# Kernel tuning notes

Measured on AMD Instinct MI355X. Metric: run time of the kernel, lower is better.

The kernel has to match this reference:

```python
import jax, jax.numpy as jnp
import numpy as np

H = 1024       # hidden_size
E = 1024       # embedding_size
V = 50257      # output_size (vocab)
L = 64         # max_length


def setup_inputs() -> dict:
    key = jax.random.key(0)
    ks = jax.random.split(key, 12)
    s = 0.02
    return {
        "input": jax.random.randint(ks[0], (1,), 0, V),
        "hidden": jax.random.normal(ks[1], (1, 1, H), dtype=jnp.float32),
        "encoder_outputs": jax.random.normal(ks[2], (L, H), dtype=jnp.float32),
        "emb": jax.random.normal(ks[3], (V, E), dtype=jnp.float32) * s,
        "attn_w": jax.random.normal(ks[4], (L, H + E), dtype=jnp.float32) * s,
        "attn_b": jnp.zeros((L,), dtype=jnp.float32),
        "comb_w": jax.random.normal(ks[5], (E, H + E), dtype=jnp.float32) * s,
        "comb_b": jnp.zeros((E,), dtype=jnp.float32),
        "w_ih": jax.random.normal(ks[6], (3 * H, E), dtype=jnp.float32) * s,
        "b_ih": jnp.zeros((3 * H,), dtype=jnp.float32),
        "w_hh": jax.random.normal(ks[7], (3 * H, H), dtype=jnp.float32) * s,
        "b_hh": jnp.zeros((3 * H,), dtype=jnp.float32),
        "out_w": jax.random.normal(ks[8], (V, H), dtype=jnp.float32) * s,
        "out_b": jnp.zeros((V,), dtype=jnp.float32),
    }


def reference(input, hidden, encoder_outputs, emb, attn_w, attn_b,
              comb_w, comb_b, w_ih, b_ih, w_hh, b_hh, out_w, out_b):
    # embedding + (dropout = identity in eval)
    embedded = emb[input].reshape(1, E)            # [1, E]
    h0 = hidden[0]                                  # [1, H]
    # Bahdanau-style attention over fixed-length encoder outputs
    attn_logits = jnp.concatenate([embedded, h0], axis=1) @ attn_w.T + attn_b
    attn_weights = jax.nn.softmax(attn_logits, axis=1)      # [1, L]
    attn_applied = attn_weights @ encoder_outputs            # [1, H]
    x = jnp.concatenate([embedded, attn_applied], axis=1) @ comb_w.T + comb_b
    x = jax.nn.relu(x)                               # [1, E]
    # single GRU cell step (torch gate order: r, z, n)
    gi = x @ w_ih.T + b_ih
    gh = h0 @ w_hh.T + b_hh
    i_r, i_z, i_n = jnp.split(gi, 3, axis=1)
    h_r, h_z, h_n = jnp.split(gh, 3, axis=1)
    r = jax.nn.sigmoid(i_r + h_r)
    z = jax.nn.sigmoid(i_z + h_z)
    n = jnp.tanh(i_n + r * h_n)
    h_new = (1.0 - z) * n + z * h0                   # [1, H]
    logp = jax.nn.log_softmax(h_new @ out_w.T + out_b, axis=1)  # [1, V]
    return logp, h_new[None], attn_weights
```

## Files before the change

### kernel.cpp

```cpp
#include <hip/hip_runtime.h>
#include <math.h>

#define H 1024
#define E 1024
#define V 50257
#define L 64
#define HE 2048

__device__ inline float wave_reduce_sum(float v) {
    #pragma unroll
    for (int off = 32; off > 0; off >>= 1)
        v += __shfl_down(v, off, 64);
    return v;
}

__device__ inline float wave_allreduce_sum(float v) {
    #pragma unroll
    for (int off = 32; off > 0; off >>= 1)
        v += __shfl_xor(v, off, 64);
    return v;
}

__device__ inline void ms_merge(float& M, float& S, float m2, float s2) {
    if (s2 > 0.f) {
        if (m2 > M) { S = S * expf(M - m2) + s2; M = m2; }
        else        { S += s2 * expf(m2 - M); }
    }
}

__global__ __launch_bounds__(1024) void k_attn_fused(
        const int* __restrict__ inp,
        const float* __restrict__ hidden,
        const float* __restrict__ emb,
        const float* __restrict__ attn_w,
        const float* __restrict__ attn_b,
        const float* __restrict__ enc,
        float* __restrict__ attn_applied,
        float* __restrict__ out_weights) {
    __shared__ float lg[L];
    __shared__ float wsm[L];
    int t = threadIdx.x;
    int wave = t >> 6, lane = t & 63;
    const float* erow = emb + (size_t)inp[0] * E;
    const float4* e4 = (const float4*)erow;
    const float4* h4 = (const float4*)hidden;
    #pragma unroll
    for (int r = wave; r < L; r += 16) {
        const float4* w = (const float4*)(attn_w + (size_t)r * HE);
        float s = 0.f;
        #pragma unroll
        for (int i = 0; i < 4; ++i) {
            float4 wv = w[i * 64 + lane];
            float4 ev = e4[i * 64 + lane];
            s += wv.x*ev.x + wv.y*ev.y + wv.z*ev.z + wv.w*ev.w;
        }
        #pragma unroll
        for (int i = 0; i < 4; ++i) {
            float4 wv = w[256 + i * 64 + lane];
            float4 hv = h4[i * 64 + lane];
            s += wv.x*hv.x + wv.y*hv.y + wv.z*hv.z + wv.w*hv.w;
        }
        s = wave_reduce_sum(s);
        if (lane == 0) lg[r] = s + attn_b[r];
    }
    __syncthreads();
    if (t < 64) {
        float v = lg[t];
        float m = v;
        #pragma unroll
        for (int off = 32; off > 0; off >>= 1) m = fmaxf(m, __shfl_xor(m, off, 64));
        float ex = expf(v - m);
        float ssum = ex;
        #pragma unroll
        for (int off = 32; off > 0; off >>= 1) ssum += __shfl_xor(ssum, off, 64);
        float w = ex / ssum;
        wsm[t] = w;
        out_weights[t] = w;
    }
    __syncthreads();
    float acc = 0.f;
    #pragma unroll 16
    for (int l = 0; l < L; ++l)
        acc += wsm[l] * enc[l * H + t];
    attn_applied[t] = acc;
}

__global__ __launch_bounds__(256) void k_comb(
        const int* __restrict__ inp,
        const float* __restrict__ emb,
        const float* __restrict__ attn_applied,
        const float* __restrict__ comb_w,
        const float* __restrict__ comb_b,
        float* __restrict__ x) {
    int t = threadIdx.x, wave = t >> 6, lane = t & 63;
    int row  = blockIdx.x * 2 + (wave >> 1);
    int half = wave & 1;
    const float* erow = emb + (size_t)inp[0] * E;
    const float4* vec = half ? (const float4*)attn_applied : (const float4*)erow;
    const float4* w = (const float4*)(comb_w + (size_t)row * HE + half * E);
    float s = 0.f;
    #pragma unroll
    for (int i = 0; i < 4; ++i) {
        float4 wv = w[i * 64 + lane];
        float4 vv = vec[i * 64 + lane];
        s += wv.x*vv.x + wv.y*vv.y + wv.z*vv.z + wv.w*vv.w;
    }
    s = wave_reduce_sum(s);
    __shared__ float red[4];
    if (lane == 0) red[wave] = s;
    __syncthreads();
    if (t < 2) {
        int r = blockIdx.x * 2 + t;
        x[r] = fmaxf(red[2 * t] + red[2 * t + 1] + comb_b[r], 0.f);
    }
}

__global__ __launch_bounds__(384) void k_gru(
        const float* __restrict__ x,
        const float* __restrict__ hidden,
        const float* __restrict__ w_ih,
        const float* __restrict__ b_ih,
        const float* __restrict__ w_hh,
        const float* __restrict__ b_hh,
        float* __restrict__ h_new) {
    int t = threadIdx.x, wave = t >> 6, lane = t & 63;
    int j = blockIdx.x;
    const float* W    = (wave < 3) ? w_ih : w_hh;
    const float* vsrc = (wave < 3) ? x    : hidden;
    int g = (wave < 3) ? wave : wave - 3;
    const float4* wr = (const float4*)(W + (size_t)(g * H + j) * H);
    const float4* v4 = (const float4*)vsrc;
    float s = 0.f;
    #pragma unroll
    for (int i = 0; i < 4; ++i) {
        float4 wv = wr[i * 64 + lane];
        float4 vv = v4[i * 64 + lane];
        s += wv.x*vv.x + wv.y*vv.y + wv.z*vv.z + wv.w*vv.w;
    }
    s = wave_reduce_sum(s);
    __shared__ float red[6];
    if (lane == 0) red[wave] = s;
    __syncthreads();
    if (t == 0) {
        float i_r = red[0] + b_ih[j];
        float i_z = red[1] + b_ih[H + j];
        float i_n = red[2] + b_ih[2 * H + j];
        float h_r = red[3] + b_hh[j];
        float h_z = red[4] + b_hh[H + j];
        float h_n = red[5] + b_hh[2 * H + j];
        float r = 1.f / (1.f + expf(-(i_r + h_r)));
        float z = 1.f / (1.f + expf(-(i_z + h_z)));
        float n = tanhf(i_n + r * h_n);
        h_new[j] = (1.f - z) * n + z * hidden[j];
    }
}

__global__ __launch_bounds__(256) void k_outproj(
        const float* __restrict__ h_new,
        const float* __restrict__ out_w,
        const float* __restrict__ out_b,
        float* __restrict__ logits,
        float2* __restrict__ partials) {
    int t = threadIdx.x, wave = t >> 6, lane = t & 63;
    int row0 = blockIdx.x * 16 + wave * 4;
    const float4* h4 = (const float4*)h_new;
    float4 hv[4];
    #pragma unroll
    for (int i = 0; i < 4; ++i) hv[i] = h4[i * 64 + lane];
    float M = -INFINITY, S = 0.f;
    #pragma unroll
    for (int rr = 0; rr < 4; ++rr) {
        int row = row0 + rr;
        if (row < V) {
            const float4* w = (const float4*)(out_w + (size_t)row * H);
            float s = 0.f;
            #pragma unroll
            for (int i = 0; i < 4; ++i) {
                float4 wv = w[i * 64 + lane];
                s += wv.x*hv[i].x + wv.y*hv[i].y + wv.z*hv[i].z + wv.w*hv[i].w;
            }
            s = wave_allreduce_sum(s);
            s += out_b[row];
            if (lane == 0) logits[row] = s;
            if (s > M) { S = S * expf(M - s) + 1.f; M = s; }
            else       { S += expf(s - M); }
        }
    }
    __shared__ float sm[4], ss[4];
    if (lane == 0) { sm[wave] = M; ss[wave] = S; }
    __syncthreads();
    if (t == 0) {
        #pragma unroll
        for (int i = 1; i < 4; ++i) ms_merge(sm[0], ss[0], sm[i], ss[i]);
        partials[blockIdx.x] = make_float2(sm[0], ss[0]);
    }
}

__global__ __launch_bounds__(256) void k_logsoftmax(
        float* __restrict__ logp,
        const float2* __restrict__ partials, int nb) {
    int t = threadIdx.x;
    float M = -INFINITY, S = 0.f;
    for (int i = t; i < nb; i += 256) {
        float2 p = partials[i];
        ms_merge(M, S, p.x, p.y);
    }
    #pragma unroll
    for (int off = 32; off > 0; off >>= 1) {
        float m2 = __shfl_down(M, off, 64);
        float s2 = __shfl_down(S, off, 64);
        ms_merge(M, S, m2, s2);
    }
    __shared__ float sm[4], ss[4];
    __shared__ float lz;
    if ((t & 63) == 0) { sm[t >> 6] = M; ss[t >> 6] = S; }
    __syncthreads();
    if (t == 0) {
        #pragma unroll
        for (int i = 1; i < 4; ++i) ms_merge(sm[0], ss[0], sm[i], ss[i]);
        lz = sm[0] + logf(ss[0]);
    }
    __syncthreads();
    int i = blockIdx.x * 256 + t;
    if (i < V) logp[i] -= lz;
}

extern "C" void kernel_launch(void* const* d_in, const int* in_sizes, int n_in,
                              void* d_out, int out_size, void* d_ws, size_t ws_size,
                              hipStream_t stream) {
    const int*   inp     = (const int*)d_in[0];
    const float* hidden  = (const float*)d_in[1];
    const float* enc     = (const float*)d_in[2];
    const float* emb     = (const float*)d_in[3];
    const float* attn_w  = (const float*)d_in[4];
    const float* attn_b  = (const float*)d_in[5];
    const float* comb_w  = (const float*)d_in[6];
    const float* comb_b  = (const float*)d_in[7];
    const float* w_ih    = (const float*)d_in[8];
    const float* b_ih    = (const float*)d_in[9];
    const float* w_hh    = (const float*)d_in[10];
    const float* b_hh    = (const float*)d_in[11];
    const float* out_w   = (const float*)d_in[12];
    const float* out_b   = (const float*)d_in[13];

    float* out          = (float*)d_out;
    float* logp         = out;
    float* h_new        = out + V;
    float* attn_weights = out + V + H;

    float* ws           = (float*)d_ws;
    float* attn_applied = ws;
    float* x            = ws + 1024;
    const int nb = (V + 15) / 16;
    float2* partials    = (float2*)(ws + 2048);

    k_attn_fused<<<1, 1024, 0, stream>>>(inp, hidden, emb, attn_w, attn_b,
                                         enc, attn_applied, attn_weights);
    k_comb<<<512, 256, 0, stream>>>(inp, emb, attn_applied, comb_w, comb_b, x);
    k_gru<<<1024, 384, 0, stream>>>(x, hidden, w_ih, b_ih, w_hh, b_hh, h_new);
    k_outproj<<<nb, 256, 0, stream>>>(h_new, out_w, out_b, logp, partials);
    k_logsoftmax<<<(V + 255) / 256, 256, 0, stream>>>(logp, partials, nb);
}
```

Baseline: 75.46 us.

## Precompute comb_w·enc and W_hh·h in a wide pre-kernel to shorten serial chain

The single-block attention kernel and the separate comb and GRU kernels are replaced by one wide pre-kernel. It computes the attention logits, the hidden-side GRU gates, the embedding half of the combine projection, and a comb_w × encoder_outputs product (PT) that does not depend on the softmax. A small kernel then applies the softmax and reassociates attn_weights·enc·comb_w as a 64-term weighted sum over PT. The GRU kernel now computes only the input-side gates, and the vocab projection uses 8 rows per block instead of 16. This removes the serial single-block phase and overlaps the independent matvecs, at the cost of extra FLOPs and a 256 KB workspace intermediate.

```diff
diff --git a/kernel.cpp b/kernel.cpp
--- a/kernel.cpp
+++ b/kernel.cpp
@@ -7,6 +7,10 @@
 #define L 64
 #define HE 2048
 
+__device__ inline float dot4(float4 a, float4 b) {
+    return a.x*b.x + a.y*b.y + a.z*b.z + a.w*b.w;
+}
+
 __device__ inline float wave_reduce_sum(float v) {
     #pragma unroll
     for (int off = 32; off > 0; off >>= 1)
@@ -14,13 +18,6 @@
     return v;
 }
 
-__device__ inline float wave_allreduce_sum(float v) {
-    #pragma unroll
-    for (int off = 32; off > 0; off >>= 1)
-        v += __shfl_xor(v, off, 64);
-    return v;
-}
-
 __device__ inline void ms_merge(float& M, float& S, float m2, float s2) {
     if (s2 > 0.f) {
         if (m2 > M) { S = S * expf(M - m2) + s2; M = m2; }
@@ -28,42 +25,100 @@
     }
 }
 
-__global__ __launch_bounds__(1024) void k_attn_fused(
+__global__ __launch_bounds__(256) void k_pre(
         const int* __restrict__ inp,
         const float* __restrict__ hidden,
+        const float* __restrict__ enc,
         const float* __restrict__ emb,
         const float* __restrict__ attn_w,
         const float* __restrict__ attn_b,
-        const float* __restrict__ enc,
-        float* __restrict__ attn_applied,
-        float* __restrict__ out_weights) {
-    __shared__ float lg[L];
-    __shared__ float wsm[L];
-    int t = threadIdx.x;
-    int wave = t >> 6, lane = t & 63;
+        const float* __restrict__ comb_w,
+        const float* __restrict__ w_hh,
+        const float* __restrict__ b_hh,
+        float* __restrict__ lg,
+        float* __restrict__ gh,
+        float* __restrict__ q1,
+        float* __restrict__ PT) {
+    const int bid  = blockIdx.x;
+    const int t    = threadIdx.x;
+    const int wave = t >> 6;
+    const int lane = t & 63;
+    __shared__ float red[4];
+
     const float* erow = emb + (size_t)inp[0] * E;
     const float4* e4 = (const float4*)erow;
     const float4* h4 = (const float4*)hidden;
-    #pragma unroll
-    for (int r = wave; r < L; r += 16) {
-        const float4* w = (const float4*)(attn_w + (size_t)r * HE);
+
+    if (bid < 64) {
+        const float4* w = (const float4*)(attn_w + (size_t)bid * HE);
+        float4 w1 = w[t];
+        float4 ev = e4[t];
+        float4 w2 = w[256 + t];
+        float4 hv = h4[t];
+        float s = dot4(w1, ev) + dot4(w2, hv);
+        s = wave_reduce_sum(s);
+        if (lane == 0) red[wave] = s;
+        __syncthreads();
+        if (t == 0) lg[bid] = red[0] + red[1] + red[2] + red[3] + attn_b[bid];
+    } else if (bid < 832) {
+        int row = (bid - 64) * 4 + wave;
+        const float4* wr = (const float4*)(w_hh + (size_t)row * H);
         float s = 0.f;
         #pragma unroll
-        for (int i = 0; i < 4; ++i) {
-            float4 wv = w[i * 64 + lane];
-            float4 ev = e4[i * 64 + lane];
-            s += wv.x*ev.x + wv.y*ev.y + wv.z*ev.z + wv.w*ev.w;
-        }
-        #pragma unroll
-        for (int i = 0; i < 4; ++i) {
-            float4 wv = w[256 + i * 64 + lane];
-            float4 hv = h4[i * 64 + lane];
-            s += wv.x*hv.x + wv.y*hv.y + wv.z*hv.z + wv.w*hv.w;
-        }
+        for (int i = 0; i < 4; ++i)
+            s += dot4(wr[i * 64 + lane], h4[i * 64 + lane]);
         s = wave_reduce_sum(s);
-        if (lane == 0) lg[r] = s + attn_b[r];
-    }
-    __syncthreads();
+        if (lane == 0) gh[row] = s + b_hh[row];
+    } else if (bid < 1088) {
+        int row = (bid - 832) * 4 + wave;
+        const float4* wr = (const float4*)(comb_w + (size_t)row * HE);
+        float s = 0.f;
+        #pragma unroll
+        for (int i = 0; i < 4; ++i)
+            s += dot4(wr[i * 64 + lane], e4[i * 64 + lane]);
+        s = wave_reduce_sum(s);
+        if (lane == 0) q1[row] = s;
+    } else {
+        int r0 = (bid - 1088) * 16 + wave * 4;
+        float4 wreg[4][4];
+        #pragma unroll
+        for (int rr = 0; rr < 4; ++rr) {
+            const float4* wr = (const float4*)(comb_w + (size_t)(r0 + rr) * HE + E);
+            #pragma unroll
+            for (int i = 0; i < 4; ++i) wreg[rr][i] = wr[i * 64 + lane];
+        }
+        const float4* enc4 = (const float4*)enc;
+        for (int l = 0; l < L; ++l) {
+            float s0 = 0.f, s1 = 0.f, s2 = 0.f, s3 = 0.f;
+            #pragma unroll
+            for (int i = 0; i < 4; ++i) {
+                float4 ev = enc4[l * 256 + i * 64 + lane];
+                s0 += dot4(wreg[0][i], ev);
+                s1 += dot4(wreg[1][i], ev);
+                s2 += dot4(wreg[2][i], ev);
+                s3 += dot4(wreg[3][i], ev);
+            }
+            s0 = wave_reduce_sum(s0);
+            s1 = wave_reduce_sum(s1);
+            s2 = wave_reduce_sum(s2);
+            s3 = wave_reduce_sum(s3);
+            if (lane == 0) {
+                float* p = PT + l * 1024 + r0;
+                p[0] = s0; p[1] = s1; p[2] = s2; p[3] = s3;
+            }
+        }
+    }
+}
+
+__global__ __launch_bounds__(256) void k_comb2(
+        const float* __restrict__ lg,
+        const float* __restrict__ q1,
+        const float* __restrict__ PT,
+        const float* __restrict__ comb_b,
+        float* __restrict__ x,
+        float* __restrict__ out_weights) {
+    __shared__ float ssig[L];
+    int t = threadIdx.x;
     if (t < 64) {
         float v = lg[t];
         float m = v;
@@ -74,125 +129,103 @@
         #pragma unroll
         for (int off = 32; off > 0; off >>= 1) ssum += __shfl_xor(ssum, off, 64);
         float w = ex / ssum;
-        wsm[t] = w;
-        out_weights[t] = w;
-    }
-    __syncthreads();
-    float acc = 0.f;
+        ssig[t] = w;
+        if (blockIdx.x == 0) out_weights[t] = w;
+    }
+    __syncthreads();
+    int r = blockIdx.x * 256 + t;
+    float acc = q1[r];
     #pragma unroll 16
     for (int l = 0; l < L; ++l)
-        acc += wsm[l] * enc[l * H + t];
-    attn_applied[t] = acc;
-}
-
-__global__ __launch_bounds__(256) void k_comb(
-        const int* __restrict__ inp,
-        const float* __restrict__ emb,
-        const float* __restrict__ attn_applied,
-        const float* __restrict__ comb_w,
-        const float* __restrict__ comb_b,
-        float* __restrict__ x) {
-    int t = threadIdx.x, wave = t >> 6, lane = t & 63;
-    int row  = blockIdx.x * 2 + (wave >> 1);
-    int half = wave & 1;
-    const float* erow = emb + (size_t)inp[0] * E;
-    const float4* vec = half ? (const float4*)attn_applied : (const float4*)erow;
-    const float4* w = (const float4*)(comb_w + (size_t)row * HE + half * E);
-    float s = 0.f;
-    #pragma unroll
-    for (int i = 0; i < 4; ++i) {
-        float4 wv = w[i * 64 + lane];
-        float4 vv = vec[i * 64 + lane];
-        s += wv.x*vv.x + wv.y*vv.y + wv.z*vv.z + wv.w*vv.w;
-    }
-    s = wave_reduce_sum(s);
-    __shared__ float red[4];
-    if (lane == 0) red[wave] = s;
-    __syncthreads();
-    if (t < 2) {
-        int r = blockIdx.x * 2 + t;
-        x[r] = fmaxf(red[2 * t] + red[2 * t + 1] + comb_b[r], 0.f);
-    }
-}
-
-__global__ __launch_bounds__(384) void k_gru(
+        acc += ssig[l] * PT[l * 1024 + r];
+    x[r] = fmaxf(acc + comb_b[r], 0.f);
+}
+
+__global__ __launch_bounds__(384) void k_gru2(
         const float* __restrict__ x,
         const float* __restrict__ hidden,
         const float* __restrict__ w_ih,
         const float* __restrict__ b_ih,
-        const float* __restrict__ w_hh,
-        const float* __restrict__ b_hh,
+        const float* __restrict__ gh,
         float* __restrict__ h_new) {
     int t = threadIdx.x, wave = t >> 6, lane = t & 63;
-    int j = blockIdx.x;
-    const float* W    = (wave < 3) ? w_ih : w_hh;
-    const float* vsrc = (wave < 3) ? x    : hidden;
-    int g = (wave < 3) ? wave : wave - 3;
-    const float4* wr = (const float4*)(W + (size_t)(g * H + j) * H);
-    const float4* v4 = (const float4*)vsrc;
+    int jj = wave / 3;
+    int g  = wave - 3 * jj;
+    int j  = blockIdx.x * 2 + jj;
+    const float4* x4 = (const float4*)x;
+    const float4* wr = (const float4*)(w_ih + (size_t)(g * H + j) * E);
     float s = 0.f;
     #pragma unroll
-    for (int i = 0; i < 4; ++i) {
-        float4 wv = wr[i * 64 + lane];
-        float4 vv = v4[i * 64 + lane];
-        s += wv.x*vv.x + wv.y*vv.y + wv.z*vv.z + wv.w*vv.w;
-    }
+    for (int i = 0; i < 4; ++i)
+        s += dot4(wr[i * 64 + lane], x4[i * 64 + lane]);
     s = wave_reduce_sum(s);
-    __shared__ float red[6];
-    if (lane == 0) red[wave] = s;
-    __syncthreads();
-    if (t == 0) {
-        float i_r = red[0] + b_ih[j];
-        float i_z = red[1] + b_ih[H + j];
-        float i_n = red[2] + b_ih[2 * H + j];
-        float h_r = red[3] + b_hh[j];
-        float h_z = red[4] + b_hh[H + j];
-        float h_n = red[5] + b_hh[2 * H + j];
+    __shared__ float red[2][3];
+    if (lane == 0) red[jj][g] = s + b_ih[g * H + j];
+    __syncthreads();
+    if (t < 2) {
+        int jo = blockIdx.x * 2 + t;
+        float i_r = red[t][0], i_z = red[t][1], i_n = red[t][2];
+        float h_r = gh[jo], h_z = gh[H + jo], h_n = gh[2 * H + jo];
         float r = 1.f / (1.f + expf(-(i_r + h_r)));
         float z = 1.f / (1.f + expf(-(i_z + h_z)));
         float n = tanhf(i_n + r * h_n);
-        h_new[j] = (1.f - z) * n + z * hidden[j];
-    }
-}
-
-__global__ __launch_bounds__(256) void k_outproj(
+        h_new[jo] = (1.f - z) * n + z * hidden[jo];
+    }
+}
+
+__global__ __launch_bounds__(256) void k_vocab(
         const float* __restrict__ h_new,
         const float* __restrict__ out_w,
         const float* __restrict__ out_b,
-        float* __restrict__ logits,
+        float* __restrict__ logp,
         float2* __restrict__ partials) {
     int t = threadIdx.x, wave = t >> 6, lane = t & 63;
-    int row0 = blockIdx.x * 16 + wave * 4;
     const float4* h4 = (const float4*)h_new;
     float4 hv[4];
     #pragma unroll
     for (int i = 0; i < 4; ++i) hv[i] = h4[i * 64 + lane];
-    float M = -INFINITY, S = 0.f;
-    #pragma unroll
-    for (int rr = 0; rr < 4; ++rr) {
-        int row = row0 + rr;
-        if (row < V) {
-            const float4* w = (const float4*)(out_w + (size_t)row * H);
-            float s = 0.f;
+    int r0 = blockIdx.x * 8 + wave * 2;
+    int r1 = r0 + 1;
+    float s0 = 0.f, s1 = 0.f;
+    if (r0 < V) {
+        const float4* w0 = (const float4*)(out_w + (size_t)r0 * H);
+        const float4* w1 = (const float4*)(out_w + (size_t)r1 * H);
+        bool v1 = r1 < V;
+        #pragma unroll
+        for (int i = 0; i < 4; ++i) s0 += dot4(w0[i * 64 + lane], hv[i]);
+        if (v1) {
             #pragma unroll
-            for (int i = 0; i < 4; ++i) {
-                float4 wv = w[i * 64 + lane];
-                s += wv.x*hv[i].x + wv.y*hv[i].y + wv.z*hv[i].z + wv.w*hv[i].w;
+            for (int i = 0; i < 4; ++i) s1 += dot4(w1[i * 64 + lane], hv[i]);
+        }
+        #pragma unroll
+        for (int off = 32; off > 0; off >>= 1) {
+            s0 += __shfl_down(s0, off, 64);
+            s1 += __shfl_down(s1, off, 64);
+        }
+    }
+    __shared__ float smM[4], smS[4];
+    if (lane == 0) {
+        float M = -INFINITY, S = 0.f;
+        if (r0 < V) {
+            s0 += out_b[r0];
+            logp[r0] = s0;
+            M = s0; S = 1.f;
+            if (r1 < V) {
+                s1 += out_b[r1];
+                logp[r1] = s1;
+                float nm = fmaxf(M, s1);
+                S = S * expf(M - nm) + expf(s1 - nm);
+                M = nm;
             }
-            s = wave_allreduce_sum(s);
-            s += out_b[row];
-            if (lane == 0) logits[row] = s;
-            if (s > M) { S = S * expf(M - s) + 1.f; M = s; }
-            else       { S += expf(s - M); }
-        }
-    }
-    __shared__ float sm[4], ss[4];
-    if (lane == 0) { sm[wave] = M; ss[wave] = S; }
+        }
+        smM[wave] = M; smS[wave] = S;
+    }
     __syncthreads();
     if (t == 0) {
-        #pragma unroll
-        for (int i = 1; i < 4; ++i) ms_merge(sm[0], ss[0], sm[i], ss[i]);
-        partials[blockIdx.x] = make_float2(sm[0], ss[0]);
+        float Mb = smM[0], Sb = smS[0];
+        #pragma unroll
+        for (int i = 1; i < 4; ++i) ms_merge(Mb, Sb, smM[i], smS[i]);
+        partials[blockIdx.x] = make_float2(Mb, Sb);
     }
 }
 
@@ -212,15 +245,16 @@
         ms_merge(M, S, m2, s2);
     }
     __shared__ float sm[4], ss[4];
-    __shared__ float lz;
+    __shared__ float sh_lz;
     if ((t & 63) == 0) { sm[t >> 6] = M; ss[t >> 6] = S; }
     __syncthreads();
     if (t == 0) {
         #pragma unroll
         for (int i = 1; i < 4; ++i) ms_merge(sm[0], ss[0], sm[i], ss[i]);
-        lz = sm[0] + logf(ss[0]);
-    }
-    __syncthreads();
+        sh_lz = sm[0] + logf(ss[0]);
+    }
+    __syncthreads();
+    float lz = sh_lz;
     int i = blockIdx.x * 256 + t;
     if (i < V) logp[i] -= lz;
 }
@@ -248,16 +282,19 @@
     float* h_new        = out + V;
     float* attn_weights = out + V + H;
 
-    float* ws           = (float*)d_ws;
-    float* attn_applied = ws;
-    float* x            = ws + 1024;
-    const int nb = (V + 15) / 16;
-    float2* partials    = (float2*)(ws + 2048);
-
-    k_attn_fused<<<1, 1024, 0, stream>>>(inp, hidden, emb, attn_w, attn_b,
-                                         enc, attn_applied, attn_weights);
-    k_comb<<<512, 256, 0, stream>>>(inp, emb, attn_applied, comb_w, comb_b, x);
-    k_gru<<<1024, 384, 0, stream>>>(x, hidden, w_ih, b_ih, w_hh, b_hh, h_new);
-    k_outproj<<<nb, 256, 0, stream>>>(h_new, out_w, out_b, logp, partials);
+    float* ws  = (float*)d_ws;
+    float* lg  = ws;
+    float* gh  = ws + 64;
+    float* q1  = ws + 3136;
+    float* x   = ws + 4160;
+    float* PT  = ws + 5184;
+    float2* partials = (float2*)(ws + 70720);
+    const int nb = (V + 7) / 8;
+
+    k_pre<<<1152, 256, 0, stream>>>(inp, hidden, enc, emb, attn_w, attn_b,
+                                    comb_w, w_hh, b_hh, lg, gh, q1, PT);
+    k_comb2<<<4, 256, 0, stream>>>(lg, q1, PT, comb_b, x, attn_weights);
+    k_gru2<<<512, 384, 0, stream>>>(x, hidden, w_ih, b_ih, gh, h_new);
+    k_vocab<<<nb, 256, 0, stream>>>(h_new, out_w, out_b, logp, partials);
     k_logsoftmax<<<(V + 255) / 256, 256, 0, stream>>>(logp, partials, nb);
 }
```

Measured after the change: 100.9 us. 1.34x slower.
